# Optimization experiments

Measured on AMD Instinct MI355X. Metric: run time of the kernel, lower is better.

The kernel has to match this reference:

```python
import jax, jax.numpy as jnp
import numpy as np

STRIDES = (4, 8, 16, 32, 64, 128)
MAPS = (128, 64, 32, 16, 8, 4)
VAR0, VAR1 = 0.1, 0.2
CLS_TH, NMS_TH, FINAL_TH = 0.05, 0.3, 0.5


def _decode_scale(ocls, oreg, stride):
    # ocls: [1,2,H,W], oreg: [1,4,H,W] -> dets [H*W, 5] = (x1,y1,x2,y2,score)
    prob = jax.nn.softmax(ocls, axis=1)[0, 1]          # [H,W] face probability
    H, W = prob.shape
    s = jnp.float32(stride)
    pcx = s / 2 + jnp.arange(W, dtype=jnp.float32)[None, :] * s   # prior center x
    pcy = s / 2 + jnp.arange(H, dtype=jnp.float32)[:, None] * s   # prior center y
    pwh = s * 4.0                                                 # prior w = h = 4*stride
    loc = oreg[0]                                                 # [4,H,W]
    cx = pcx + loc[0] * VAR0 * pwh
    cy = pcy + loc[1] * VAR0 * pwh
    w = pwh * jnp.exp(loc[2] * VAR1)
    h = pwh * jnp.exp(loc[3] * VAR1)
    x1 = cx - w / 2
    y1 = cy - h / 2
    x2 = x1 + w
    y2 = y1 + h
    return jnp.stack([x1.ravel(), y1.ravel(), x2.ravel(), y2.ravel(), prob.ravel()], axis=1)


def _nms_keep(dets, valid):
    # Greedy NMS (torch-style, +1 box convention), fixed trip count, returns keep mask.
    N = dets.shape[0]
    scores = jnp.where(valid, dets[:, 4], -jnp.inf)
    order = jnp.argsort(-scores)            # descending by score, invalid last
    b = dets[order]
    v = valid[order]
    x1, y1, x2, y2 = b[:, 0], b[:, 1], b[:, 2], b[:, 3]
    areas = (x2 - x1 + 1.0) * (y2 - y1 + 1.0)
    pos = jnp.arange(N)

    def body(i, carry):
        sup, keep = carry
        active = jnp.logical_and(jnp.logical_not(sup[i]), v[i])
        keep = keep.at[i].set(active)
        xx1 = jnp.maximum(x1[i], x1)
        yy1 = jnp.maximum(y1[i], y1)
        xx2 = jnp.minimum(x2[i], x2)
        yy2 = jnp.minimum(y2[i], y2)
        w = jnp.maximum(xx2 - xx1 + 1.0, 0.0)
        h = jnp.maximum(yy2 - yy1 + 1.0, 0.0)
        inter = w * h
        iou = inter / (areas[i] + areas - inter)
        sup = sup | (active & (iou > NMS_TH) & (pos > i))
        return sup, keep

    sup0 = jnp.logical_not(v)
    _, keep_sorted = jax.lax.fori_loop(0, N, body, (sup0, jnp.zeros(N, dtype=bool)))
    return jnp.zeros(N, dtype=bool).at[order].set(keep_sorted)


def _forward(ol1, ol2, ol3, ol4, ol5, ol6, ol7, ol8, ol9, ol10, ol11, ol12):
    olist = [ol1, ol2, ol3, ol4, ol5, ol6, ol7, ol8, ol9, ol10, ol11, ol12]
    dets = jnp.concatenate(
        [_decode_scale(olist[2 * i], olist[2 * i + 1], STRIDES[i]) for i in range(6)],
        axis=0)                              # [N,5]
    valid = dets[:, 4] > CLS_TH              # threshold stage (score > 0.05)
    # NMS selection is index logic -> constant w.r.t. differentiation
    keep = _nms_keep(jax.lax.stop_gradient(dets), valid)
    final = keep & (dets[:, 4] > FINAL_TH)   # post-NMS score > 0.5 filter
    # fixed-shape equivalent of gathering kept rows: zero out non-kept rows
    return dets * final[:, None].astype(dets.dtype)


def setup_inputs() -> dict:
    key = jax.random.key(0)
    inp = {}
    for i, hw in enumerate(MAPS):
        kc, kr, key = jax.random.split(key, 3)
        inp[f"ol{2 * i + 1}"] = jax.random.normal(kc, (1, 2, hw, hw), dtype=jnp.float32)
        inp[f"ol{2 * i + 2}"] = jax.random.normal(kr, (1, 4, hw, hw), dtype=jnp.float32)
    return inp


def reference(ol1, ol2, ol3, ol4, ol5, ol6, ol7, ol8, ol9, ol10, ol11, ol12):
    return _forward(ol1, ol2, ol3, ol4, ol5, ol6, ol7, ol8, ol9, ol10, ol11, ol12)
```

## Files before the change

kernel.cpp:

```cpp
#include <hip/hip_runtime.h>
#include <stdint.h>

#define N_TOTAL 21840
#define NA      21888
#define W_MAX   342
#define TOT_ENT 3753792u
#define NMS_TH  0.3f
#define FINAL_TH 0.5f
#define NSLICE  8
#define SCAN_T  768
#define NPUSH   11
#define PLANES  704
#define GRP     4
#define NBAND   7
#define GMAX    86

struct Inputs { const float* cls[6]; const float* reg[6]; };

__device__ __forceinline__ void block_bar() {
  asm volatile("s_waitcnt lgkmcnt(0)\n\ts_barrier" ::: "memory");
}

__device__ __forceinline__ unsigned wbase_u(unsigned w) {
  return 64u * (342u * w - (w * (w - 1u)) / 2u);
}

__global__ void decode_kernel(Inputs in,
                              float* __restrict__ dx1, float* __restrict__ dy1,
                              float* __restrict__ dx2, float* __restrict__ dy2,
                              float* __restrict__ dsc,
                              unsigned long long* __restrict__ ckey,
                              unsigned int* __restrict__ Mc,
                              unsigned int* __restrict__ rank32,
                              unsigned int* __restrict__ wcnt,
                              float* __restrict__ out) {
#pragma clang fp contract(off)
  int gid = blockIdx.x * blockDim.x + threadIdx.x;
  if (gid >= N_TOTAL) return;

  rank32[gid] = 0u;
  wcnt[gid] = 0u;
  if (gid < NA - N_TOTAL) wcnt[N_TOTAL + gid] = 0u;

  int sc, local;
  if      (gid < 16384) { sc = 0; local = gid;         }
  else if (gid < 20480) { sc = 1; local = gid - 16384; }
  else if (gid < 21504) { sc = 2; local = gid - 20480; }
  else if (gid < 21760) { sc = 3; local = gid - 21504; }
  else if (gid < 21824) { sc = 4; local = gid - 21760; }
  else                  { sc = 5; local = gid - 21824; }

  const int Wd     = 128 >> sc;
  const int stride = 4 << sc;
  const int HW     = Wd * Wd;
  const int x = local & (Wd - 1);
  const int y = local >> (7 - sc);

  const float* cls = in.cls[sc];
  const float* reg = in.reg[sc];

  float c0 = cls[local];
  float c1 = cls[HW + local];
  float m  = fmaxf(c0, c1);
  float e0 = expf(c0 - m);
  float e1 = expf(c1 - m);
  float prob = e1 / (e0 + e1);

  float l0 = reg[local];
  float l1 = reg[HW + local];
  float l2 = reg[2 * HW + local];
  float l3 = reg[3 * HW + local];

  float sF  = (float)stride;
  float pcx = 0.5f * sF + (float)x * sF;
  float pcy = 0.5f * sF + (float)y * sF;
  float pwh = sF * 4.0f;

  float cx = pcx + ((l0 * 0.1f) * pwh);
  float cy = pcy + ((l1 * 0.1f) * pwh);
  float w  = pwh * expf(l2 * 0.2f);
  float h  = pwh * expf(l3 * 0.2f);
  float x1 = cx - w * 0.5f;
  float y1 = cy - h * 0.5f;
  float x2 = x1 + w;
  float y2 = y1 + h;

  dx1[gid] = x1; dy1[gid] = y1; dx2[gid] = x2; dy2[gid] = y2; dsc[gid] = prob;

  out[gid * 5 + 0] = 0.0f;
  out[gid * 5 + 1] = 0.0f;
  out[gid * 5 + 2] = 0.0f;
  out[gid * 5 + 3] = 0.0f;
  out[gid * 5 + 4] = 0.0f;

  if (prob > FINAL_TH) {
    unsigned int pos = atomicAdd(Mc, 1u);
    ckey[pos] = ((unsigned long long)__float_as_uint(prob) << 32) |
                (unsigned int)(~(unsigned int)gid);
  }
}

__global__ void __launch_bounds__(256)
rank_kernel(const unsigned long long* __restrict__ ckey,
            const unsigned int* __restrict__ Mc,
            const float* __restrict__ dx1, const float* __restrict__ dy1,
            const float* __restrict__ dx2, const float* __restrict__ dy2,
            float* __restrict__ sx1, float* __restrict__ sy1,
            float* __restrict__ sx2, float* __restrict__ sy2,
            unsigned int* __restrict__ sorig,
            unsigned int* __restrict__ rank32) {
  __shared__ unsigned long long tile[256];
  const unsigned int M = *Mc;
  if (blockIdx.x * 256u >= M) return;
  const int t = (int)threadIdx.x;
  const int p = (int)blockIdx.x * 256 + t;
  unsigned long long mykey = (p < (int)M) ? ckey[p] : 0ull;
  const int S  = (int)((M + NSLICE - 1) / NSLICE);
  const int lo = (int)blockIdx.y * S;
  const int hi = min((int)M, lo + S);
  int partial = 0;
  const int nt = (hi > lo) ? ((hi - lo + 255) >> 8) : 0;
  for (int ti = 0; ti < nt; ++ti) {
    int j = lo + ti * 256 + t;
    tile[t] = (j < hi) ? ckey[j] : 0ull;
    __syncthreads();
#pragma unroll 8
    for (int q = 0; q < 256; ++q) partial += (tile[q] > mykey) ? 1 : 0;
    __syncthreads();
  }
  if (p < (int)M) {
    unsigned int pack = (unsigned int)partial | (1u << 24);
    unsigned int old  = atomicAdd(&rank32[p], pack);
    unsigned int newv = old + pack;
    if ((newv >> 24) == NSLICE) {
      int r = (int)(newv & 0xFFFFFF);
      unsigned int orig = ~(unsigned int)(mykey & 0xffffffffull);
      sx1[r] = dx1[orig];
      sy1[r] = dy1[orig];
      sx2[r] = dx2[orig];
      sy2[r] = dy2[orig];
      sorig[r] = orig;
    }
  }
}

__global__ void __launch_bounds__(1024)
pairs_kernel(const float* __restrict__ sx1, const float* __restrict__ sy1,
             const float* __restrict__ sx2, const float* __restrict__ sy2,
             const unsigned int* __restrict__ Mc,
             unsigned long long* __restrict__ diag,
             unsigned long long* __restrict__ bandT,
             unsigned int* __restrict__ wcnt,
             unsigned short* __restrict__ rlMeta,
             unsigned long long* __restrict__ rlBits) {
#pragma clang fp contract(off)
  const int M = (int)*Mc;
  const int W = (M + 63) >> 6;
  const int rw = (int)blockIdx.y;
  const int cwg = (int)blockIdx.x << 4;
  if (rw >= W || cwg >= W || cwg + 22 < rw) return;

  const int t = (int)threadIdx.x;
  const int g = t >> 6, l = t & 63;
  const int cw = cwg + g;

  __shared__ float cx1[1024], cy1[1024], cx2[1024], cy2[1024], car[1024];
  __shared__ unsigned wvcnt[16], wvbase[16];
  {
    int c = (cw << 6) + l;
    if (cw < W && c < M) {
      float a = sx1[c], b = sy1[c], d = sx2[c], e = sy2[c];
      cx1[t] = a; cy1[t] = b; cx2[t] = d; cy2[t] = e;
      car[t] = (d - a + 1.0f) * (e - b + 1.0f);
    }
  }
  __syncthreads();

  const int rwg = rw >> 2, cg = cw >> 2;
  const bool inW    = (cw < W);
  const bool isDiag = inW && (cw == rw);
  const bool isBand = inW && (cw < rw) && (cg >= rwg - 1);
  const bool isCsr  = inW && (cg >= rwg + 2);
  const bool any    = isDiag || isBand || isCsr;

  const int r = (rw << 6) + l;
  unsigned long long bits = 0ull;
  if (any && r < M) {
    float ax1 = sx1[r], ay1 = sy1[r], ax2 = sx2[r], ay2 = sy2[r];
    float aarea = (ax2 - ax1 + 1.0f) * (ay2 - ay1 + 1.0f);
    const int cmax = min(64, M - (cw << 6));
    const int sb = g << 6;
    for (int cc = 0; cc < cmax; ++cc) {
      float xx1 = fmaxf(ax1, cx1[sb + cc]);
      float yy1 = fmaxf(ay1, cy1[sb + cc]);
      float xx2 = fminf(ax2, cx2[sb + cc]);
      float yy2 = fminf(ay2, cy2[sb + cc]);
      float ww = fmaxf(xx2 - xx1 + 1.0f, 0.0f);
      float hh = fmaxf(yy2 - yy1 + 1.0f, 0.0f);
      float inter = ww * hh;
      float iou = inter / (aarea + car[sb + cc] - inter);
      if (iou > NMS_TH) bits |= (1ull << cc);
    }
  }
  if (isDiag)      diag[r] = bits;
  else if (isBand) bandT[(size_t)(rw - cw - 1) * NA + r] = bits;

  unsigned long long ball = 0ull;
  unsigned myrank = 0u;
  {
    bool mine = isCsr && (bits != 0ull);
    ball = __ballot(mine);
    myrank = (unsigned)__popcll(ball & ((1ull << l) - 1ull));
    if (l == 0) wvcnt[g] = (unsigned)__popcll(ball);
  }
  __syncthreads();
  if (t == 0) {
    unsigned tot = 0u;
    unsigned pre[16];
#pragma unroll
    for (int i = 0; i < 16; ++i) { pre[i] = tot; tot += wvcnt[i]; }
    unsigned base = (tot != 0u) ? atomicAdd(&wcnt[rw], tot) : 0u;
#pragma unroll
    for (int i = 0; i < 16; ++i) wvbase[i] = base + pre[i];
  }
  __syncthreads();
  if (isCsr && bits != 0ull) {
    unsigned slot = wbase_u((unsigned)rw) + wvbase[g] + myrank;
    rlMeta[slot] = (unsigned short)(((unsigned)l << 9) | (unsigned)cw);
    rlBits[slot] = bits;
  }
}

__global__ void __launch_bounds__(SCAN_T, 3)
scan_kernel(const unsigned long long* __restrict__ diag,
            const unsigned long long* __restrict__ bandT,
            const unsigned int* __restrict__ wcnt,
            const unsigned short* __restrict__ rlMeta,
            const unsigned long long* __restrict__ rlBits,
            const unsigned int* __restrict__ sorig,
            const unsigned int* __restrict__ Mc,
            const float* __restrict__ dx1, const float* __restrict__ dy1,
            const float* __restrict__ dx2, const float* __restrict__ dy2,
            const float* __restrict__ dsc,
            float* __restrict__ out) {
  __shared__ unsigned long long sup[W_MAX];
  __shared__ unsigned long long kmls[W_MAX];
  __shared__ unsigned lds_wcnt[W_MAX];
  __shared__ unsigned gdone[GMAX];
  __shared__ volatile unsigned sflag;
  const int t = (int)threadIdx.x;
  const int g = t >> 6, l = t & 63;
  const int M = (int)*Mc;
  const int W = (M + 63) >> 6;
  const int NS = (W + 3) >> 2;

  for (int i = t; i < W_MAX; i += SCAN_T) {
    sup[i] = 0ull; kmls[i] = 0ull; lds_wcnt[i] = wcnt[i];
  }
  for (int i = t; i < GMAX; i += SCAN_T) gdone[i] = 0u;
  if (t == 0) sflag = 0u;
  block_bar();

  if (g == 0) {
    __builtin_amdgcn_s_setprio(1);
    const unsigned long long lowm = (1ull << l) - 1ull;
    unsigned long long dc[4], dn[4];
    unsigned long long bc[4][NBAND], bn[4][NBAND];
    unsigned long long kp[4] = {0ull, 0ull, 0ull, 0ull};
#pragma unroll
    for (int i = 0; i < 4; ++i) {
      int v = i, vc = (v < W) ? v : 0;
      dc[i] = diag[(vc << 6) + l];
#pragma unroll
      for (int d = 1; d <= NBAND; ++d)
        if (d <= i + 4) bc[i][d - 1] = bandT[(size_t)(d - 1) * NA + (vc << 6) + l];
    }
#pragma unroll
    for (int i = 0; i < 4; ++i) {
      int v = 4 + i, vc = (v < W) ? v : 0;
      dn[i] = diag[(vc << 6) + l];
#pragma unroll
      for (int d = 1; d <= NBAND; ++d)
        if (d <= i + 4) bn[i][d - 1] = bandT[(size_t)(d - 1) * NA + (vc << 6) + l];
    }
    for (int s = 0; s < NS; ++s) {
      const int v0 = s << 2;
      unsigned long long accp[4];
#pragma unroll
      for (int i = 0; i < 4; ++i) {
        unsigned long long a = 0ull;
#pragma unroll
        for (int d = 1; d <= NBAND; ++d)
          if (d <= i + 4 && d > i) a |= (bc[i][d - 1] & kp[i - d + 4]);
        accp[i] = a;
      }
      if (s >= 2) {
        while (*(volatile unsigned*)&gdone[s - 2] < (unsigned)NPUSH) {}
        asm volatile("" ::: "memory");
      }
      unsigned long long sv[4];
#pragma unroll
      for (int i = 0; i < 4; ++i)
        sv[i] = (v0 + i < W) ? sup[v0 + i] : 0ull;
      unsigned long long kc[4];
#pragma unroll
      for (int i = 0; i < 4; ++i) {
        const int v = v0 + i;
        unsigned long long kept = 0ull;
        if (v < W) {
          unsigned long long acc = accp[i];
#pragma unroll
          for (int d = 1; d <= 3; ++d)
            if (d <= i) acc |= (bc[i][d - 1] & kc[i - d]);
          unsigned long long incoming = __ballot(acc != 0ull);
          const int n = min(64, M - (v << 6));
          unsigned long long wm = (n >= 64) ? ~0ull : ((1ull << n) - 1ull);
          unsigned long long pend = (~(sv[i] | incoming)) & wm;
          const unsigned long long dv = dc[i] & lowm;
          unsigned long long dead = ~pend, und = pend;
          while (und) {
            unsigned long long bS = __ballot((dv & kept) != 0ull) & und;
            unsigned long long bK = __ballot((dv & ~dead) == 0ull) & und;
            kept |= bK; dead |= bS; und &= ~(bK | bS);
          }
          if (l == i) kmls[v] = kept;
        }
        kc[i] = kept;
      }
      asm volatile("s_waitcnt lgkmcnt(0)" ::: "memory");
      if (l == 0) sflag = (unsigned)(s + 1);
#pragma unroll
      for (int i = 0; i < 4; ++i) kp[i] = kc[i];
#pragma unroll
      for (int i = 0; i < 4; ++i) {
        dc[i] = dn[i];
#pragma unroll
        for (int d = 0; d < NBAND; ++d)
          if (d <= i + 3) bc[i][d] = bn[i][d];
      }
      const int vn = v0 + 8;
#pragma unroll
      for (int i = 0; i < 4; ++i) {
        int v = vn + i, vc = (v < W) ? v : 0;
        dn[i] = diag[(vc << 6) + l];
#pragma unroll
        for (int d = 1; d <= NBAND; ++d)
          if (d <= i + 4) bn[i][d - 1] = bandT[(size_t)(d - 1) * NA + (vc << 6) + l];
      }
    }
    __builtin_amdgcn_s_setprio(0);
  } else {
    const int p = (g - 1) * 64 + l;

#define PUSH_LOAD(mX, bX, gs)                                               \
    {                                                                       \
      _Pragma("unroll")                                                     \
      for (int i = 0; i < 4; ++i) {                                         \
        int v = (gs) * 4 + i;                                               \
        unsigned vc = (v < W) ? (unsigned)v : 0u;                           \
        unsigned base = wbase_u(vc);                                        \
        unsigned i0 = base + (unsigned)p;   if (i0 >= TOT_ENT) i0 = 0u;     \
        unsigned i1 = i0 + (unsigned)PLANES; if (i1 >= TOT_ENT) i1 = 0u;    \
        mX[i][0] = (unsigned)rlMeta[i0]; bX[i][0] = rlBits[i0];             \
        mX[i][1] = (unsigned)rlMeta[i1]; bX[i][1] = rlBits[i1];             \
      }                                                                     \
    }

    unsigned mA[4][2], mB[4][2];
    unsigned long long bA[4][2], bB[4][2];
    PUSH_LOAD(mA, bA, 0)
    PUSH_LOAD(mB, bB, 1)
    for (int s = 0; s < NS; ++s) {
      while (sflag < (unsigned)(s + 1)) __builtin_amdgcn_s_sleep(1);
      asm volatile("" ::: "memory");
#pragma unroll
      for (int i = 0; i < 4; ++i) {
        const int v = (s << 2) + i;
        if (v < W) {
          const unsigned tw = lds_wcnt[v];
          const unsigned long long km = kmls[v];
          if (km != 0ull && tw != 0u) {
            if ((unsigned)p < tw && ((km >> (mA[i][0] >> 9)) & 1ull))
              atomicOr(&sup[mA[i][0] & 511u], bA[i][0]);
            if ((unsigned)p + (unsigned)PLANES < tw &&
                ((km >> (mA[i][1] >> 9)) & 1ull))
              atomicOr(&sup[mA[i][1] & 511u], bA[i][1]);
            if (tw > 2u * (unsigned)PLANES) {
              unsigned base = wbase_u((unsigned)v);
              for (unsigned ii = (unsigned)p + 2u * (unsigned)PLANES;
                   ii < tw; ii += (unsigned)PLANES) {
                unsigned sl = base + ii; if (sl >= TOT_ENT) sl = TOT_ENT - 1u;
                unsigned mm = (unsigned)rlMeta[sl];
                if ((km >> (mm >> 9)) & 1ull)
                  atomicOr(&sup[mm & 511u], rlBits[sl]);
              }
            }
          }
        }
      }
      asm volatile("s_waitcnt lgkmcnt(0)" ::: "memory");
      if (l == 0) atomicAdd(&gdone[s], 1u);
#pragma unroll
      for (int i = 0; i < 4; ++i) {
        mA[i][0] = mB[i][0]; mA[i][1] = mB[i][1];
        bA[i][0] = bB[i][0]; bA[i][1] = bB[i][1];
      }
      PUSH_LOAD(mB, bB, s + 2)
    }
#undef PUSH_LOAD
  }
  block_bar();

  for (int i = t; i < (W << 6); i += SCAN_T) {
    if ((kmls[i >> 6] >> (i & 63)) & 1ull) {
      unsigned int orig = sorig[i];
      out[(size_t)orig * 5 + 0] = dx1[orig];
      out[(size_t)orig * 5 + 1] = dy1[orig];
      out[(size_t)orig * 5 + 2] = dx2[orig];
      out[(size_t)orig * 5 + 3] = dy2[orig];
      out[(size_t)orig * 5 + 4] = dsc[orig];
    }
  }
}

__global__ void __launch_bounds__(1024)
nms_kernel(const float* __restrict__ sx1, const float* __restrict__ sy1,
           const float* __restrict__ sx2, const float* __restrict__ sy2,
           const unsigned int* __restrict__ sorig,
           const unsigned int* __restrict__ Mc,
           unsigned int* __restrict__ keepflag) {
#pragma clang fp contract(off)
  __shared__ unsigned long long sup[W_MAX];
  __shared__ unsigned long long inrow[64];
  __shared__ float wx1[64], wy1[64], wx2[64], wy2[64], warea[64];
  __shared__ unsigned long long keptmask_sh;

  const int t = (int)threadIdx.x;
  const int M = (int)*Mc;
  const int W = (M + 63) >> 6;

  for (int i = t; i < W_MAX; i += 1024) sup[i] = 0ull;
  __syncthreads();

  for (int w = 0; w < W; ++w) {
    const int base = w << 6;
    const int n = min(64, M - base);
    if (t < 64) {
      if (t < n) {
        float a = sx1[base + t], b = sy1[base + t];
        float c = sx2[base + t], d = sy2[base + t];
        wx1[t] = a; wy1[t] = b; wx2[t] = c; wy2[t] = d;
        warea[t] = (c - a + 1.0f) * (d - b + 1.0f);
      }
    } else if (t < 128) {
      inrow[t - 64] = 0ull;
    }
    __syncthreads();
    {
      int r = t & 63, seg = t >> 6;
      unsigned long long bits = 0ull;
      if (r < n) {
        float ax1 = wx1[r], ay1 = wy1[r], ax2 = wx2[r], ay2 = wy2[r];
        float aarea = warea[r];
        for (int c = seg * 4; c < seg * 4 + 4; ++c) {
          if (c > r && c < n) {
            float xx1 = fmaxf(ax1, wx1[c]);
            float yy1 = fmaxf(ay1, wy1[c]);
            float xx2 = fminf(ax2, wx2[c]);
            float yy2 = fminf(ay2, wy2[c]);
            float ww = fmaxf(xx2 - xx1 + 1.0f, 0.0f);
            float hh = fmaxf(yy2 - yy1 + 1.0f, 0.0f);
            float inter = ww * hh;
            float iou = inter / (aarea + warea[c] - inter);
            if (iou > NMS_TH) bits |= (1ull << c);
          }
        }
      }
      if (bits) atomicOr(&inrow[r], bits);
    }
    __syncthreads();
    if (t < 64) {
      unsigned long long wordmask = (n >= 64) ? ~0ull : ((1ull << n) - 1ull);
      unsigned long long pending = (~sup[w]) & wordmask;
      unsigned long long kept = 0ull;
      while (pending) {
        int i = __builtin_ctzll(pending);
        kept |= (1ull << i);
        pending &= ~(inrow[i] | (1ull << i));
      }
      if (t == 0) keptmask_sh = kept;
      if (t < n && ((kept >> t) & 1ull)) keepflag[sorig[base + t]] = 1u;
    }
    __syncthreads();
    unsigned long long km = keptmask_sh;
    if (km) {
      int wid = t >> 6, lane = t & 63;
      for (int jw = w + 1 + wid; (jw << 6) < M; jw += 16) {
        int j = (jw << 6) + lane;
        bool supj = false;
        if (j < M) {
          float jx1 = sx1[j], jy1 = sy1[j], jx2 = sx2[j], jy2 = sy2[j];
          float jarea = (jx2 - jx1 + 1.0f) * (jy2 - jy1 + 1.0f);
          unsigned long long mm = km;
          while (mm) {
            int r = __builtin_ctzll(mm);
            mm &= mm - 1ull;
            float xx1 = fmaxf(wx1[r], jx1);
            float yy1 = fmaxf(wy1[r], jy1);
            float xx2 = fminf(wx2[r], jx2);
            float yy2 = fminf(wy2[r], jy2);
            float ww = fmaxf(xx2 - xx1 + 1.0f, 0.0f);
            float hh = fmaxf(yy2 - yy1 + 1.0f, 0.0f);
            float inter = ww * hh;
            float iou = inter / (warea[r] + jarea - inter);
            if (iou > NMS_TH) { supj = true; break; }
          }
        }
        unsigned long long bal = __ballot(supj);
        if (lane == 0 && bal) atomicOr(&sup[jw], bal);
      }
    }
    __syncthreads();
  }
}

__global__ void output_kernel(const float* __restrict__ dx1, const float* __restrict__ dy1,
                              const float* __restrict__ dx2, const float* __restrict__ dy2,
                              const float* __restrict__ dsc,
                              const unsigned int* __restrict__ keepflag,
                              float* __restrict__ out) {
#pragma clang fp contract(off)
  int gid = blockIdx.x * blockDim.x + threadIdx.x;
  if (gid >= N_TOTAL) return;
  float f = keepflag[gid] ? 1.0f : 0.0f;
  out[gid * 5 + 0] = dx1[gid] * f;
  out[gid * 5 + 1] = dy1[gid] * f;
  out[gid * 5 + 2] = dx2[gid] * f;
  out[gid * 5 + 3] = dy2[gid] * f;
  out[gid * 5 + 4] = dsc[gid] * f;
}

extern "C" void kernel_launch(void* const* d_in, const int* in_sizes, int n_in,
                              void* d_out, int out_size, void* d_ws, size_t ws_size,
                              hipStream_t stream) {
  (void)in_sizes; (void)n_in; (void)out_size;

  Inputs in;
  for (int i = 0; i < 6; ++i) {
    in.cls[i] = (const float*)d_in[2 * i];
    in.reg[i] = (const float*)d_in[2 * i + 1];
  }

  char* ws = (char*)d_ws;
  size_t o = 0;
  float* dx1 = (float*)(ws + o); o += (size_t)NA * 4;
  float* dy1 = (float*)(ws + o); o += (size_t)NA * 4;
  float* dx2 = (float*)(ws + o); o += (size_t)NA * 4;
  float* dy2 = (float*)(ws + o); o += (size_t)NA * 4;
  float* dsc = (float*)(ws + o); o += (size_t)NA * 4;
  unsigned long long* ckey = (unsigned long long*)(ws + o); o += (size_t)NA * 8;
  float* sx1 = (float*)(ws + o); o += (size_t)NA * 4;
  float* sy1 = (float*)(ws + o); o += (size_t)NA * 4;
  float* sx2 = (float*)(ws + o); o += (size_t)NA * 4;
  float* sy2 = (float*)(ws + o); o += (size_t)NA * 4;
  unsigned int* sorig = (unsigned int*)(ws + o); o += (size_t)NA * 4;
  unsigned int* keepflag = (unsigned int*)(ws + o); o += (size_t)NA * 4;
  unsigned int* rank32 = (unsigned int*)(ws + o); o += (size_t)NA * 4;
  unsigned int* wcnt = (unsigned int*)(ws + o); o += (size_t)NA * 4;
  unsigned int* Mc = (unsigned int*)(ws + o); o += 64;
  o = (o + 511) & ~(size_t)511;
  unsigned long long* diag = (unsigned long long*)(ws + o); o += (size_t)NA * 8;
  unsigned long long* bandT = (unsigned long long*)(ws + o); o += (size_t)NBAND * NA * 8;
  unsigned long long* rlBits = (unsigned long long*)(ws + o); o += (size_t)TOT_ENT * 8;
  unsigned short* rlMeta = (unsigned short*)(ws + o); o += (size_t)TOT_ENT * 2;
  size_t need = o;
  const bool fast = (need <= ws_size);

  const int nb = (N_TOTAL + 255) / 256;

  if (fast) {
    (void)hipMemsetAsync((void*)Mc, 0, 64, stream);
    decode_kernel<<<nb, 256, 0, stream>>>(in, dx1, dy1, dx2, dy2, dsc, ckey, Mc,
                                          rank32, wcnt, (float*)d_out);
    rank_kernel<<<dim3(nb, NSLICE), 256, 0, stream>>>(ckey, Mc, dx1, dy1, dx2, dy2,
                                                      sx1, sy1, sx2, sy2, sorig,
                                                      rank32);
    pairs_kernel<<<dim3(22, W_MAX), 1024, 0, stream>>>(sx1, sy1, sx2, sy2, Mc,
                                                       diag, bandT, wcnt, rlMeta, rlBits);
    scan_kernel<<<1, SCAN_T, 0, stream>>>(diag, bandT, wcnt, rlMeta, rlBits, sorig, Mc,
                                          dx1, dy1, dx2, dy2, dsc, (float*)d_out);
  } else {
    (void)hipMemsetAsync((void*)keepflag, 0, (size_t)NA * 12 + 64, stream);
    decode_kernel<<<nb, 256, 0, stream>>>(in, dx1, dy1, dx2, dy2, dsc, ckey, Mc,
                                          rank32, wcnt, (float*)d_out);
    rank_kernel<<<dim3(nb, NSLICE), 256, 0, stream>>>(ckey, Mc, dx1, dy1, dx2, dy2,
                                                      sx1, sy1, sx2, sy2, sorig,
                                                      rank32);
    nms_kernel<<<1, 1024, 0, stream>>>(sx1, sy1, sx2, sy2, sorig, Mc, keepflag);
    output_kernel<<<nb, 256, 0, stream>>>(dx1, dy1, dx2, dy2, dsc, keepflag,
                                          (float*)d_out);
  }
}
```

Measured before the change: 261.6 us.

## Widen NMS scan groups from 4 to 8 words with a 15-word band

Doubles the group of 64-box words handled per scan step from 4 to 8 and widens the dense band of intra-group suppression masks from 7 to 15 words. The pairs kernel and the push warps change to match. This halves the number of handshakes between the serial scan wave and the push waves. The scan wave also drops its double-buffered register prefetch of diag and band masks and now loads them at the start of each step. That adds load latency on the serial critical path and raises register pressure, since 8x15 band registers are live plus 8x2 push buffers.

```diff
diff --git a/kernel.cpp b/kernel.cpp
--- a/kernel.cpp
+++ b/kernel.cpp
@@ -11,9 +11,9 @@
 #define SCAN_T  768
 #define NPUSH   11
 #define PLANES  704
-#define GRP     4
-#define NBAND   7
-#define GMAX    86
+#define GRP     8
+#define NBAND   15
+#define GMAX    43
 
 struct Inputs { const float* cls[6]; const float* reg[6]; };
 
@@ -158,7 +158,7 @@
   const int W = (M + 63) >> 6;
   const int rw = (int)blockIdx.y;
   const int cwg = (int)blockIdx.x << 4;
-  if (rw >= W || cwg >= W || cwg + 22 < rw) return;
+  if (rw >= W || cwg >= W || cwg + 30 < rw) return;
 
   const int t = (int)threadIdx.x;
   const int g = t >> 6, l = t & 63;
@@ -176,7 +176,7 @@
   }
   __syncthreads();
 
-  const int rwg = rw >> 2, cg = cw >> 2;
+  const int rwg = rw >> 3, cg = cw >> 3;
   const bool inW    = (cw < W);
   const bool isDiag = inW && (cw == rw);
   const bool isBand = inW && (cw < rw) && (cg >= rwg - 1);
@@ -252,7 +252,7 @@
   const int g = t >> 6, l = t & 63;
   const int M = (int)*Mc;
   const int W = (M + 63) >> 6;
-  const int NS = (W + 3) >> 2;
+  const int NS = (W + 7) >> 3;
 
   for (int i = t; i < W_MAX; i += SCAN_T) {
     sup[i] = 0ull; kmls[i] = 0ull; lds_wcnt[i] = wcnt[i];
@@ -264,59 +264,52 @@
   if (g == 0) {
     __builtin_amdgcn_s_setprio(1);
     const unsigned long long lowm = (1ull << l) - 1ull;
-    unsigned long long dc[4], dn[4];
-    unsigned long long bc[4][NBAND], bn[4][NBAND];
-    unsigned long long kp[4] = {0ull, 0ull, 0ull, 0ull};
-#pragma unroll
-    for (int i = 0; i < 4; ++i) {
-      int v = i, vc = (v < W) ? v : 0;
-      dc[i] = diag[(vc << 6) + l];
-#pragma unroll
-      for (int d = 1; d <= NBAND; ++d)
-        if (d <= i + 4) bc[i][d - 1] = bandT[(size_t)(d - 1) * NA + (vc << 6) + l];
-    }
-#pragma unroll
-    for (int i = 0; i < 4; ++i) {
-      int v = 4 + i, vc = (v < W) ? v : 0;
-      dn[i] = diag[(vc << 6) + l];
-#pragma unroll
-      for (int d = 1; d <= NBAND; ++d)
-        if (d <= i + 4) bn[i][d - 1] = bandT[(size_t)(d - 1) * NA + (vc << 6) + l];
-    }
+    unsigned long long kp[8] = {0ull,0ull,0ull,0ull,0ull,0ull,0ull,0ull};
     for (int s = 0; s < NS; ++s) {
-      const int v0 = s << 2;
-      unsigned long long accp[4];
-#pragma unroll
-      for (int i = 0; i < 4; ++i) {
-        unsigned long long a = 0ull;
+      const int v0 = s << 3;
+      unsigned long long dg[8];
+      unsigned long long bd[8][NBAND];
+#pragma unroll
+      for (int i = 0; i < 8; ++i) {
+        int v = v0 + i, vc = (v < W) ? v : 0;
+        dg[i] = diag[(vc << 6) + l];
 #pragma unroll
         for (int d = 1; d <= NBAND; ++d)
-          if (d <= i + 4 && d > i) a |= (bc[i][d - 1] & kp[i - d + 4]);
-        accp[i] = a;
+          if (d <= i + 8)
+            bd[i][d - 1] = bandT[(size_t)(d - 1) * NA + (vc << 6) + l];
       }
       if (s >= 2) {
         while (*(volatile unsigned*)&gdone[s - 2] < (unsigned)NPUSH) {}
         asm volatile("" ::: "memory");
       }
-      unsigned long long sv[4];
-#pragma unroll
-      for (int i = 0; i < 4; ++i)
+      unsigned long long accp[8];
+#pragma unroll
+      for (int i = 0; i < 8; ++i) {
+        unsigned long long a = 0ull;
+#pragma unroll
+        for (int d = 1; d <= NBAND; ++d)
+          if (d <= i + 8 && d > i) a |= (bd[i][d - 1] & kp[i - d + 8]);
+        accp[i] = a;
+      }
+      unsigned long long sv[8];
+#pragma unroll
+      for (int i = 0; i < 8; ++i)
         sv[i] = (v0 + i < W) ? sup[v0 + i] : 0ull;
-      unsigned long long kc[4];
-#pragma unroll
-      for (int i = 0; i < 4; ++i) {
+      unsigned long long kc[8];
+#pragma unroll
+      for (int i = 0; i < 8; ++i) {
         const int v = v0 + i;
         unsigned long long kept = 0ull;
         if (v < W) {
           unsigned long long acc = accp[i];
 #pragma unroll
-          for (int d = 1; d <= 3; ++d)
-            if (d <= i) acc |= (bc[i][d - 1] & kc[i - d]);
+          for (int d = 1; d <= 7; ++d)
+            if (d <= i) acc |= (bd[i][d - 1] & kc[i - d]);
           unsigned long long incoming = __ballot(acc != 0ull);
           const int n = min(64, M - (v << 6));
           unsigned long long wm = (n >= 64) ? ~0ull : ((1ull << n) - 1ull);
           unsigned long long pend = (~(sv[i] | incoming)) & wm;
-          const unsigned long long dv = dc[i] & lowm;
+          const unsigned long long dv = dg[i] & lowm;
           unsigned long long dead = ~pend, und = pend;
           while (und) {
             unsigned long long bS = __ballot((dv & kept) != 0ull) & und;
@@ -330,23 +323,7 @@
       asm volatile("s_waitcnt lgkmcnt(0)" ::: "memory");
       if (l == 0) sflag = (unsigned)(s + 1);
 #pragma unroll
-      for (int i = 0; i < 4; ++i) kp[i] = kc[i];
-#pragma unroll
-      for (int i = 0; i < 4; ++i) {
-        dc[i] = dn[i];
-#pragma unroll
-        for (int d = 0; d < NBAND; ++d)
-          if (d <= i + 3) bc[i][d] = bn[i][d];
-      }
-      const int vn = v0 + 8;
-#pragma unroll
-      for (int i = 0; i < 4; ++i) {
-        int v = vn + i, vc = (v < W) ? v : 0;
-        dn[i] = diag[(vc << 6) + l];
-#pragma unroll
-        for (int d = 1; d <= NBAND; ++d)
-          if (d <= i + 4) bn[i][d - 1] = bandT[(size_t)(d - 1) * NA + (vc << 6) + l];
-      }
+      for (int i = 0; i < 8; ++i) kp[i] = kc[i];
     }
     __builtin_amdgcn_s_setprio(0);
   } else {
@@ -355,8 +332,8 @@
 #define PUSH_LOAD(mX, bX, gs)                                               \
     {                                                                       \
       _Pragma("unroll")                                                     \
-      for (int i = 0; i < 4; ++i) {                                         \
-        int v = (gs) * 4 + i;                                               \
+      for (int i = 0; i < 8; ++i) {                                         \
+        int v = (gs) * 8 + i;                                               \
         unsigned vc = (v < W) ? (unsigned)v : 0u;                           \
         unsigned base = wbase_u(vc);                                        \
         unsigned i0 = base + (unsigned)p;   if (i0 >= TOT_ENT) i0 = 0u;     \
@@ -366,16 +343,16 @@
       }                                                                     \
     }
 
-    unsigned mA[4][2], mB[4][2];
-    unsigned long long bA[4][2], bB[4][2];
+    unsigned mA[8][2], mB[8][2];
+    unsigned long long bA[8][2], bB[8][2];
     PUSH_LOAD(mA, bA, 0)
     PUSH_LOAD(mB, bB, 1)
     for (int s = 0; s < NS; ++s) {
       while (sflag < (unsigned)(s + 1)) __builtin_amdgcn_s_sleep(1);
       asm volatile("" ::: "memory");
 #pragma unroll
-      for (int i = 0; i < 4; ++i) {
-        const int v = (s << 2) + i;
+      for (int i = 0; i < 8; ++i) {
+        const int v = (s << 3) + i;
         if (v < W) {
           const unsigned tw = lds_wcnt[v];
           const unsigned long long km = kmls[v];
@@ -401,7 +378,7 @@
       asm volatile("s_waitcnt lgkmcnt(0)" ::: "memory");
       if (l == 0) atomicAdd(&gdone[s], 1u);
 #pragma unroll
-      for (int i = 0; i < 4; ++i) {
+      for (int i = 0; i < 8; ++i) {
         mA[i][0] = mB[i][0]; mA[i][1] = mB[i][1];
         bA[i][0] = bB[i][0]; bA[i][1] = bB[i][1];
       }
```

Result: slower. 467.0 us (+78.5%).

## Fuse decode, rank, pair and scan stages into one cooperative kernel

Applied to the files above, without the earlier changes.

Replaces the memset plus four separate kernel launches with a single cooperative kernel that uses grid-wide syncs between the decode, rank, pairwise IoU mask and sequential scan phases. The goal is to remove launch overhead and inter-kernel gaps. In exchange, the later phases run on only 256 blocks via grid-stride loops, the final scan runs on block 0 while the rest exit, and grid.sync has its own cost. If the cooperative launch fails, the code falls back to the old multi-kernel path.

```diff
diff --git a/kernel.cpp b/kernel.cpp
--- a/kernel.cpp
+++ b/kernel.cpp
@@ -1,5 +1,8 @@
 #include <hip/hip_runtime.h>
+#include <hip/hip_cooperative_groups.h>
 #include <stdint.h>
+
+namespace cg = cooperative_groups;
 
 #define N_TOTAL 21840
 #define NA      21888
@@ -14,6 +17,8 @@
 #define GRP     4
 #define NBAND   7
 #define GMAX    86
+#define FUSED_B 256
+#define FUSED_T 1024
 
 struct Inputs { const float* cls[6]; const float* reg[6]; };
 
@@ -23,6 +28,407 @@
 
 __device__ __forceinline__ unsigned wbase_u(unsigned w) {
   return 64u * (342u * w - (w * (w - 1u)) / 2u);
+}
+
+__global__ void __launch_bounds__(FUSED_T, 4)
+fused_kernel(Inputs in,
+             float* __restrict__ dx1, float* __restrict__ dy1,
+             float* __restrict__ dx2, float* __restrict__ dy2,
+             float* __restrict__ dsc,
+             unsigned long long* __restrict__ ckey,
+             float* __restrict__ sx1, float* __restrict__ sy1,
+             float* __restrict__ sx2, float* __restrict__ sy2,
+             unsigned int* __restrict__ sorig,
+             unsigned int* __restrict__ rank32,
+             unsigned int* __restrict__ wcnt,
+             unsigned int* __restrict__ Mc,
+             unsigned long long* __restrict__ diag,
+             unsigned long long* __restrict__ bandT,
+             unsigned short* __restrict__ rlMeta,
+             unsigned long long* __restrict__ rlBits,
+             float* __restrict__ out) {
+#pragma clang fp contract(off)
+  cg::grid_group grid = cg::this_grid();
+  __shared__ unsigned long long smem8[2592];
+
+  const int tid = (int)threadIdx.x;
+  const int bid = (int)blockIdx.x;
+  const int gtid = bid * FUSED_T + tid;
+
+  if (gtid < 16) Mc[gtid] = 0u;
+  grid.sync();
+
+  for (int gid = gtid; gid < N_TOTAL; gid += FUSED_B * FUSED_T) {
+    rank32[gid] = 0u;
+    wcnt[gid] = 0u;
+    if (gid < NA - N_TOTAL) wcnt[N_TOTAL + gid] = 0u;
+
+    int sc, local;
+    if      (gid < 16384) { sc = 0; local = gid;         }
+    else if (gid < 20480) { sc = 1; local = gid - 16384; }
+    else if (gid < 21504) { sc = 2; local = gid - 20480; }
+    else if (gid < 21760) { sc = 3; local = gid - 21504; }
+    else if (gid < 21824) { sc = 4; local = gid - 21760; }
+    else                  { sc = 5; local = gid - 21824; }
+
+    const int Wd     = 128 >> sc;
+    const int stride = 4 << sc;
+    const int HW     = Wd * Wd;
+    const int x = local & (Wd - 1);
+    const int y = local >> (7 - sc);
+
+    const float* cls = in.cls[sc];
+    const float* reg = in.reg[sc];
+
+    float c0 = cls[local];
+    float c1 = cls[HW + local];
+    float m  = fmaxf(c0, c1);
+    float e0 = expf(c0 - m);
+    float e1 = expf(c1 - m);
+    float prob = e1 / (e0 + e1);
+
+    float l0 = reg[local];
+    float l1 = reg[HW + local];
+    float l2 = reg[2 * HW + local];
+    float l3 = reg[3 * HW + local];
+
+    float sF  = (float)stride;
+    float pcx = 0.5f * sF + (float)x * sF;
+    float pcy = 0.5f * sF + (float)y * sF;
+    float pwh = sF * 4.0f;
+
+    float cx = pcx + ((l0 * 0.1f) * pwh);
+    float cy = pcy + ((l1 * 0.1f) * pwh);
+    float w  = pwh * expf(l2 * 0.2f);
+    float h  = pwh * expf(l3 * 0.2f);
+    float x1 = cx - w * 0.5f;
+    float y1 = cy - h * 0.5f;
+    float x2 = x1 + w;
+    float y2 = y1 + h;
+
+    dx1[gid] = x1; dy1[gid] = y1; dx2[gid] = x2; dy2[gid] = y2; dsc[gid] = prob;
+
+    out[gid * 5 + 0] = 0.0f;
+    out[gid * 5 + 1] = 0.0f;
+    out[gid * 5 + 2] = 0.0f;
+    out[gid * 5 + 3] = 0.0f;
+    out[gid * 5 + 4] = 0.0f;
+
+    if (prob > FINAL_TH) {
+      unsigned int pos = atomicAdd(Mc, 1u);
+      ckey[pos] = ((unsigned long long)__float_as_uint(prob) << 32) |
+                  (unsigned int)(~(unsigned int)gid);
+    }
+  }
+  grid.sync();
+
+  {
+    unsigned long long* tile = smem8 + (size_t)(tid >> 8) * 256;
+    const unsigned int M = *Mc;
+    const int sg = tid >> 8, st = tid & 255;
+    const int unit = bid * 4 + sg;
+    const int bx = unit >> 3;
+    const int y  = unit & 7;
+    const bool live = (bx < 86);
+    const int p = bx * 256 + st;
+    unsigned long long mykey = (live && p < (int)M) ? ckey[p] : 0ull;
+    const int S  = (int)((M + NSLICE - 1) / NSLICE);
+    const int lo = y * S;
+    const int hi = min((int)M, lo + S);
+    const int ntu = (S + 255) >> 8;
+    int partial = 0;
+    for (int ti = 0; ti < ntu; ++ti) {
+      int j = lo + ti * 256 + st;
+      tile[st] = (live && j < hi) ? ckey[j] : 0ull;
+      __syncthreads();
+      if (live) {
+#pragma unroll 8
+        for (int q = 0; q < 256; ++q) partial += (tile[q] > mykey) ? 1 : 0;
+      }
+      __syncthreads();
+    }
+    if (live && p < (int)M) {
+      unsigned int pack = (unsigned int)partial | (1u << 24);
+      unsigned int old  = atomicAdd(&rank32[p], pack);
+      unsigned int newv = old + pack;
+      if ((newv >> 24) == NSLICE) {
+        int r = (int)(newv & 0xFFFFFF);
+        unsigned int orig = ~(unsigned int)(mykey & 0xffffffffull);
+        sx1[r] = dx1[orig];
+        sy1[r] = dy1[orig];
+        sx2[r] = dx2[orig];
+        sy2[r] = dy2[orig];
+        sorig[r] = orig;
+      }
+    }
+  }
+  grid.sync();
+
+  {
+    float* cx1 = (float*)smem8;
+    float* cy1 = cx1 + 1024;
+    float* cx2 = cy1 + 1024;
+    float* cy2 = cx2 + 1024;
+    float* car = cy2 + 1024;
+    unsigned* wvcnt  = (unsigned*)(car + 1024);
+    unsigned* wvbase = wvcnt + 16;
+    const int M = (int)*Mc;
+    const int W = (M + 63) >> 6;
+    const int g64 = tid >> 6, l = tid & 63;
+    for (int u = bid; u < 22 * W_MAX; u += FUSED_B) {
+      const int rw  = u / 22;
+      const int cwg = (u % 22) << 4;
+      if (rw >= W || cwg >= W || cwg + 22 < rw) continue;
+      const int cw = cwg + g64;
+      {
+        int c = (cw << 6) + l;
+        if (cw < W && c < M) {
+          float a = sx1[c], b = sy1[c], d = sx2[c], e = sy2[c];
+          cx1[tid] = a; cy1[tid] = b; cx2[tid] = d; cy2[tid] = e;
+          car[tid] = (d - a + 1.0f) * (e - b + 1.0f);
+        }
+      }
+      __syncthreads();
+
+      const int rwg = rw >> 2, cg2 = cw >> 2;
+      const bool inW    = (cw < W);
+      const bool isDiag = inW && (cw == rw);
+      const bool isBand = inW && (cw < rw) && (cg2 >= rwg - 1);
+      const bool isCsr  = inW && (cg2 >= rwg + 2);
+      const bool any    = isDiag || isBand || isCsr;
+
+      const int r = (rw << 6) + l;
+      unsigned long long bits = 0ull;
+      if (any && r < M) {
+        float ax1 = sx1[r], ay1 = sy1[r], ax2 = sx2[r], ay2 = sy2[r];
+        float aarea = (ax2 - ax1 + 1.0f) * (ay2 - ay1 + 1.0f);
+        const int cmax = min(64, M - (cw << 6));
+        const int sb = g64 << 6;
+        for (int cc = 0; cc < cmax; ++cc) {
+          float xx1 = fmaxf(ax1, cx1[sb + cc]);
+          float yy1 = fmaxf(ay1, cy1[sb + cc]);
+          float xx2 = fminf(ax2, cx2[sb + cc]);
+          float yy2 = fminf(ay2, cy2[sb + cc]);
+          float ww = fmaxf(xx2 - xx1 + 1.0f, 0.0f);
+          float hh = fmaxf(yy2 - yy1 + 1.0f, 0.0f);
+          float inter = ww * hh;
+          float iou = inter / (aarea + car[sb + cc] - inter);
+          if (iou > NMS_TH) bits |= (1ull << cc);
+        }
+      }
+      if (isDiag)      diag[r] = bits;
+      else if (isBand) bandT[(size_t)(rw - cw - 1) * NA + r] = bits;
+
+      unsigned long long ball = 0ull;
+      unsigned myrank = 0u;
+      {
+        bool mine = isCsr && (bits != 0ull);
+        ball = __ballot(mine);
+        myrank = (unsigned)__popcll(ball & ((1ull << l) - 1ull));
+        if (l == 0) wvcnt[g64] = (unsigned)__popcll(ball);
+      }
+      __syncthreads();
+      if (tid == 0) {
+        unsigned tot = 0u;
+        unsigned pre[16];
+#pragma unroll
+        for (int i = 0; i < 16; ++i) { pre[i] = tot; tot += wvcnt[i]; }
+        unsigned base = (tot != 0u) ? atomicAdd(&wcnt[rw], tot) : 0u;
+#pragma unroll
+        for (int i = 0; i < 16; ++i) wvbase[i] = base + pre[i];
+      }
+      __syncthreads();
+      if (isCsr && bits != 0ull) {
+        unsigned slot = wbase_u((unsigned)rw) + wvbase[g64] + myrank;
+        rlMeta[slot] = (unsigned short)(((unsigned)l << 9) | (unsigned)cw);
+        rlBits[slot] = bits;
+      }
+    }
+  }
+  grid.sync();
+
+  if (bid != 0) return;
+  {
+    unsigned long long* sup  = smem8;
+    unsigned long long* kmls = sup + W_MAX;
+    unsigned* lds_wcnt = (unsigned*)(kmls + W_MAX);
+    unsigned* gdone    = lds_wcnt + W_MAX;
+    unsigned* sflag_p  = gdone + GMAX;
+    const int t = tid;
+    const int g = t >> 6, l = t & 63;
+    const int M = (int)*Mc;
+    const int W = (M + 63) >> 6;
+    const int NS = (W + 3) >> 2;
+
+    for (int i = t; i < W_MAX; i += FUSED_T) {
+      sup[i] = 0ull; kmls[i] = 0ull; lds_wcnt[i] = wcnt[i];
+    }
+    for (int i = t; i < GMAX; i += FUSED_T) gdone[i] = 0u;
+    if (t == 0) *sflag_p = 0u;
+    block_bar();
+
+    if (g == 0) {
+      __builtin_amdgcn_s_setprio(1);
+      const unsigned long long lowm = (1ull << l) - 1ull;
+      unsigned long long dc[4], dn[4];
+      unsigned long long bc[4][NBAND], bn[4][NBAND];
+      unsigned long long kp[4] = {0ull, 0ull, 0ull, 0ull};
+#pragma unroll
+      for (int i = 0; i < 4; ++i) {
+        int v = i, vc = (v < W) ? v : 0;
+        dc[i] = diag[(vc << 6) + l];
+#pragma unroll
+        for (int d = 1; d <= NBAND; ++d)
+          if (d <= i + 4) bc[i][d - 1] = bandT[(size_t)(d - 1) * NA + (vc << 6) + l];
+      }
+#pragma unroll
+      for (int i = 0; i < 4; ++i) {
+        int v = 4 + i, vc = (v < W) ? v : 0;
+        dn[i] = diag[(vc << 6) + l];
+#pragma unroll
+        for (int d = 1; d <= NBAND; ++d)
+          if (d <= i + 4) bn[i][d - 1] = bandT[(size_t)(d - 1) * NA + (vc << 6) + l];
+      }
+      for (int s = 0; s < NS; ++s) {
+        const int v0 = s << 2;
+        unsigned long long accp[4];
+#pragma unroll
+        for (int i = 0; i < 4; ++i) {
+          unsigned long long a = 0ull;
+#pragma unroll
+          for (int d = 1; d <= NBAND; ++d)
+            if (d <= i + 4 && d > i) a |= (bc[i][d - 1] & kp[i - d + 4]);
+          accp[i] = a;
+        }
+        if (s >= 2) {
+          while (*(volatile unsigned*)&gdone[s - 2] < (unsigned)NPUSH) {}
+          asm volatile("" ::: "memory");
+        }
+        unsigned long long sv[4];
+#pragma unroll
+        for (int i = 0; i < 4; ++i)
+          sv[i] = (v0 + i < W) ? sup[v0 + i] : 0ull;
+        unsigned long long kc[4];
+#pragma unroll
+        for (int i = 0; i < 4; ++i) {
+          const int v = v0 + i;
+          unsigned long long kept = 0ull;
+          if (v < W) {
+            unsigned long long acc = accp[i];
+#pragma unroll
+            for (int d = 1; d <= 3; ++d)
+              if (d <= i) acc |= (bc[i][d - 1] & kc[i - d]);
+            unsigned long long incoming = __ballot(acc != 0ull);
+            const int n = min(64, M - (v << 6));
+            unsigned long long wm = (n >= 64) ? ~0ull : ((1ull << n) - 1ull);
+            unsigned long long pend = (~(sv[i] | incoming)) & wm;
+            const unsigned long long dv = dc[i] & lowm;
+            unsigned long long dead = ~pend, und = pend;
+            while (und) {
+              unsigned long long bS = __ballot((dv & kept) != 0ull) & und;
+              unsigned long long bK = __ballot((dv & ~dead) == 0ull) & und;
+              kept |= bK; dead |= bS; und &= ~(bK | bS);
+            }
+            if (l == i) kmls[v] = kept;
+          }
+          kc[i] = kept;
+        }
+        asm volatile("s_waitcnt lgkmcnt(0)" ::: "memory");
+        if (l == 0) *(volatile unsigned*)sflag_p = (unsigned)(s + 1);
+#pragma unroll
+        for (int i = 0; i < 4; ++i) kp[i] = kc[i];
+#pragma unroll
+        for (int i = 0; i < 4; ++i) {
+          dc[i] = dn[i];
+#pragma unroll
+          for (int d = 0; d < NBAND; ++d)
+            if (d <= i + 3) bc[i][d] = bn[i][d];
+        }
+        const int vn = v0 + 8;
+#pragma unroll
+        for (int i = 0; i < 4; ++i) {
+          int v = vn + i, vc = (v < W) ? v : 0;
+          dn[i] = diag[(vc << 6) + l];
+#pragma unroll
+          for (int d = 1; d <= NBAND; ++d)
+            if (d <= i + 4) bn[i][d - 1] = bandT[(size_t)(d - 1) * NA + (vc << 6) + l];
+        }
+      }
+      __builtin_amdgcn_s_setprio(0);
+    } else if (g <= NPUSH) {
+      const int p = (g - 1) * 64 + l;
+
+#define PUSH_LOAD(mX, bX, gs)                                               \
+      {                                                                     \
+        _Pragma("unroll")                                                   \
+        for (int i = 0; i < 4; ++i) {                                       \
+          int v = (gs) * 4 + i;                                             \
+          unsigned vc = (v < W) ? (unsigned)v : 0u;                         \
+          unsigned base = wbase_u(vc);                                      \
+          unsigned i0 = base + (unsigned)p;   if (i0 >= TOT_ENT) i0 = 0u;   \
+          unsigned i1 = i0 + (unsigned)PLANES; if (i1 >= TOT_ENT) i1 = 0u;  \
+          mX[i][0] = (unsigned)rlMeta[i0]; bX[i][0] = rlBits[i0];           \
+          mX[i][1] = (unsigned)rlMeta[i1]; bX[i][1] = rlBits[i1];           \
+        }                                                                   \
+      }
+
+      unsigned mA[4][2], mB[4][2];
+      unsigned long long bA[4][2], bB[4][2];
+      PUSH_LOAD(mA, bA, 0)
+      PUSH_LOAD(mB, bB, 1)
+      for (int s = 0; s < NS; ++s) {
+        while (*(volatile unsigned*)sflag_p < (unsigned)(s + 1))
+          __builtin_amdgcn_s_sleep(1);
+        asm volatile("" ::: "memory");
+#pragma unroll
+        for (int i = 0; i < 4; ++i) {
+          const int v = (s << 2) + i;
+          if (v < W) {
+            const unsigned tw = lds_wcnt[v];
+            const unsigned long long km = kmls[v];
+            if (km != 0ull && tw != 0u) {
+              if ((unsigned)p < tw && ((km >> (mA[i][0] >> 9)) & 1ull))
+                atomicOr(&sup[mA[i][0] & 511u], bA[i][0]);
+              if ((unsigned)p + (unsigned)PLANES < tw &&
+                  ((km >> (mA[i][1] >> 9)) & 1ull))
+                atomicOr(&sup[mA[i][1] & 511u], bA[i][1]);
+              if (tw > 2u * (unsigned)PLANES) {
+                unsigned base = wbase_u((unsigned)v);
+                for (unsigned ii = (unsigned)p + 2u * (unsigned)PLANES;
+                     ii < tw; ii += (unsigned)PLANES) {
+                  unsigned sl = base + ii; if (sl >= TOT_ENT) sl = TOT_ENT - 1u;
+                  unsigned mm = (unsigned)rlMeta[sl];
+                  if ((km >> (mm >> 9)) & 1ull)
+                    atomicOr(&sup[mm & 511u], rlBits[sl]);
+                }
+              }
+            }
+          }
+        }
+        asm volatile("s_waitcnt lgkmcnt(0)" ::: "memory");
+        if (l == 0) atomicAdd(&gdone[s], 1u);
+#pragma unroll
+        for (int i = 0; i < 4; ++i) {
+          mA[i][0] = mB[i][0]; mA[i][1] = mB[i][1];
+          bA[i][0] = bB[i][0]; bA[i][1] = bB[i][1];
+        }
+        PUSH_LOAD(mB, bB, s + 2)
+      }
+#undef PUSH_LOAD
+    }
+    block_bar();
+
+    for (int i = t; i < (W << 6); i += FUSED_T) {
+      if ((kmls[i >> 6] >> (i & 63)) & 1ull) {
+        unsigned int orig = sorig[i];
+        out[(size_t)orig * 5 + 0] = dx1[orig];
+        out[(size_t)orig * 5 + 1] = dy1[orig];
+        out[(size_t)orig * 5 + 2] = dx2[orig];
+        out[(size_t)orig * 5 + 3] = dy2[orig];
+        out[(size_t)orig * 5 + 4] = dsc[orig];
+      }
+    }
+  }
 }
 
 __global__ void decode_kernel(Inputs in,
@@ -579,6 +985,21 @@
   const int nb = (N_TOTAL + 255) / 256;
 
   if (fast) {
+    float* outp = (float*)d_out;
+    void* kargs[] = {
+      (void*)&in,
+      (void*)&dx1, (void*)&dy1, (void*)&dx2, (void*)&dy2, (void*)&dsc,
+      (void*)&ckey,
+      (void*)&sx1, (void*)&sy1, (void*)&sx2, (void*)&sy2,
+      (void*)&sorig, (void*)&rank32, (void*)&wcnt, (void*)&Mc,
+      (void*)&diag, (void*)&bandT, (void*)&rlMeta, (void*)&rlBits,
+      (void*)&outp
+    };
+    hipError_t e = hipLaunchCooperativeKernel(
+        (const void*)fused_kernel, dim3(FUSED_B), dim3(FUSED_T),
+        kargs, 0, stream);
+    if (e == hipSuccess) return;
+    (void)hipGetLastError();
     (void)hipMemsetAsync((void*)Mc, 0, 64, stream);
     decode_kernel<<<nb, 256, 0, stream>>>(in, dx1, dy1, dx2, dy2, dsc, ckey, Mc,
                                           rank32, wcnt, (float*)d_out);
```

New measurement: 436.4 us. 1.67x slower.
